# Optimization experiments

Hardware: AMD Instinct MI355X
Metric: run time of the kernel (lower is better)

## Reference

```python
import jax, jax.numpy as jnp
import numpy as np

H, W = 100, 100  # local_env_shape


def setup_inputs() -> dict:
    key = jax.random.key(0)
    k1, = jax.random.split(key, 1)
    B, T, P = 32, 10, 25
    # points in [0, 110): with resolution=1, origin=0 most land in the 100x100 grid,
    x = jax.random.uniform(k1, (B, T, 2 * P), dtype=jnp.float32) * 110.0
    resolution = jnp.ones((B, T, 2), dtype=jnp.float32)
    origin = jnp.zeros((B, T, 2), dtype=jnp.float32)
    return {"x": x, "resolution": resolution, "origin": origin}


def reference(x, resolution, origin):
    B, T, n = x.shape
    P = n // 2
    points = x.reshape(B, T, P, 2)  # [B, T, P, 2] (x, y)
    # row index from y-coordinate, col index from x-coordinate (cast truncates, as tf.cast does)
    row = (points[..., 1] / resolution[:, :, 0:1] + origin[:, :, 0:1]).astype(jnp.int32)  # [B,T,P]
    col = (points[..., 0] / resolution[:, :, 1:2] + origin[:, :, 1:2]).astype(jnp.int32)  # [B,T,P]
    in_bounds = (row >= 0) & (row < H) & (col >= 0) & (col < W)  # [B,T,P]
    row_safe = jnp.clip(row, 0, H - 1)
    col_safe = jnp.clip(col, 0, W - 1)
    b_idx = jnp.arange(B)[:, None, None]
    t_idx = jnp.arange(T)[None, :, None]
    p_idx = jnp.arange(P)[None, None, :]
    grid = jnp.zeros((B, T, H, W, P), dtype=jnp.float32)
    # scatter-max so masked-out (OOB) points write 0 and never clobber a valid 1
    out = grid.at[b_idx, t_idx, row_safe, col_safe, p_idx].max(in_bounds.astype(jnp.float32))
    return out
```

## Files before the change

kernel.cpp:

```cpp
#include <hip/hip_runtime.h>

#define BB 32
#define TT 10
#define PP 25
#define HH 100
#define WW 100

__global__ void raster_scatter_kernel(const float* __restrict__ x,
                                      const float* __restrict__ resolution,
                                      const float* __restrict__ origin,
                                      float* __restrict__ out) {
    int tid = blockIdx.x * blockDim.x + threadIdx.x;
    const int N = BB * TT * PP;
    if (tid >= N) return;

    int p  = tid % PP;
    int bt = tid / PP;

    const float px = x[bt * (2 * PP) + 2 * p];
    const float py = x[bt * (2 * PP) + 2 * p + 1];
    const float r0 = resolution[bt * 2 + 0];
    const float r1 = resolution[bt * 2 + 1];
    const float o0 = origin[bt * 2 + 0];
    const float o1 = origin[bt * 2 + 1];

    int row = (int)(py / r0 + o0);
    int col = (int)(px / r1 + o1);

    if (row >= 0 && row < HH && col >= 0 && col < WW) {
        size_t idx = (((size_t)bt * HH + (size_t)row) * WW + (size_t)col) * PP + (size_t)p;
        out[idx] = 1.0f;
    }
}

extern "C" void kernel_launch(void* const* d_in, const int* in_sizes, int n_in,
                              void* d_out, int out_size, void* d_ws, size_t ws_size,
                              hipStream_t stream) {
    const float* x          = (const float*)d_in[0];
    const float* resolution = (const float*)d_in[1];
    const float* origin     = (const float*)d_in[2];
    float* out = (float*)d_out;

    hipMemsetAsync(out, 0, (size_t)out_size * sizeof(float), stream);

    const int N = BB * TT * PP;
    raster_scatter_kernel<<<(N + 255) / 256, 256, 0, stream>>>(x, resolution, origin, out);
}
```

Measured before the change: 312.2 us.

## Fuse zero-fill and scatter into one kernel with nontemporal vector stores

Replaces the separate memset and scatter launch with a single kernel in which each block zeroes a chunk of one (b,t) slice using 16-byte nontemporal stores, then writes the in-bounds ones that fall inside that chunk. This removes a launch and the ordering dependency between fill and scatter. Correctness depends on the __syncthreads between the block's own zero stores and its scatter writes, since each chunk is owned by exactly one block.

```diff
diff --git a/kernel.cpp b/kernel.cpp
--- a/kernel.cpp
+++ b/kernel.cpp
@@ -6,30 +6,51 @@
 #define HH 100
 #define WW 100
 
-__global__ void raster_scatter_kernel(const float* __restrict__ x,
-                                      const float* __restrict__ resolution,
-                                      const float* __restrict__ origin,
-                                      float* __restrict__ out) {
-    int tid = blockIdx.x * blockDim.x + threadIdx.x;
-    const int N = BB * TT * PP;
-    if (tid >= N) return;
+#define SLICE4 62500
+#define CHUNKS 10
+#define CHUNK4 (SLICE4 / CHUNKS)
 
-    int p  = tid % PP;
-    int bt = tid / PP;
+typedef float floatx4 __attribute__((ext_vector_type(4)));
 
-    const float px = x[bt * (2 * PP) + 2 * p];
-    const float py = x[bt * (2 * PP) + 2 * p + 1];
-    const float r0 = resolution[bt * 2 + 0];
-    const float r1 = resolution[bt * 2 + 1];
-    const float o0 = origin[bt * 2 + 0];
-    const float o1 = origin[bt * 2 + 1];
+__global__ void raster_fused_kernel(const float* __restrict__ x,
+                                    const float* __restrict__ res,
+                                    const float* __restrict__ org,
+                                    float* __restrict__ out) {
+    const int bt    = blockIdx.y;
+    const int chunk = blockIdx.x;
+    const int t     = threadIdx.x;
 
-    int row = (int)(py / r0 + o0);
-    int col = (int)(px / r1 + o1);
+    __shared__ int tgt[PP];
+    if (t < PP) {
+        const float px = x[bt * (2 * PP) + 2 * t];
+        const float py = x[bt * (2 * PP) + 2 * t + 1];
+        const float r0 = res[bt * 2 + 0];
+        const float r1 = res[bt * 2 + 1];
+        const float o0 = org[bt * 2 + 0];
+        const float o1 = org[bt * 2 + 1];
+        const int row = (int)(py / r0 + o0);
+        const int col = (int)(px / r1 + o1);
+        tgt[t] = (row >= 0 && row < HH && col >= 0 && col < WW)
+                     ? ((row * WW + col) * PP + t)
+                     : -1;
+    }
+    __syncthreads();
 
-    if (row >= 0 && row < HH && col >= 0 && col < WW) {
-        size_t idx = (((size_t)bt * HH + (size_t)row) * WW + (size_t)col) * PP + (size_t)p;
-        out[idx] = 1.0f;
+    floatx4* dst = (floatx4*)out + (size_t)bt * SLICE4 + (size_t)chunk * CHUNK4;
+    const floatx4 z = (floatx4)(0.0f);
+    for (int i = t; i < CHUNK4; i += blockDim.x) {
+        __builtin_nontemporal_store(z, dst + i);
+    }
+
+    __syncthreads();
+
+    if (t < PP) {
+        const int g  = tgt[t];
+        const int lo = chunk * CHUNK4 * 4;
+        const int hi = lo + CHUNK4 * 4;
+        if (g >= lo && g < hi) {
+            out[(size_t)bt * SLICE4 * 4 + (size_t)g] = 1.0f;
+        }
     }
 }
 
@@ -41,8 +62,6 @@
     const float* origin     = (const float*)d_in[2];
     float* out = (float*)d_out;
 
-    hipMemsetAsync(out, 0, (size_t)out_size * sizeof(float), stream);
-
-    const int N = BB * TT * PP;
-    raster_scatter_kernel<<<(N + 255) / 256, 256, 0, stream>>>(x, resolution, origin, out);
+    dim3 grid(CHUNKS, BB * TT);
+    raster_fused_kernel<<<grid, 256, 0, stream>>>(x, resolution, origin, out);
 }
```

After: 330.0 us. +5.7%, slower.
